# Performance work log

Hardware: AMD Instinct MI355X
Metric: run time of the kernel (lower is better)

The kernel has to match this reference:

```python
import jax, jax.numpy as jnp
import numpy as np

B, L, FT, FS, H = 32, 4096, 512, 512, 512  # batch, seq, text feat, summary feat, hidden
C = FT + FS + 1  # conv1 in-channels (num_features + 1 coverage channel)


def setup_inputs() -> dict:
    key = jax.random.key(0)
    ks = jax.random.split(key, 8)
    text_states = jax.random.normal(ks[0], (B, L, FT), dtype=jnp.float32)
    summary_current_state = jax.random.normal(ks[1], (B, FS), dtype=jnp.float32)
    coverage = jax.random.uniform(ks[2], (B, 1, L), dtype=jnp.float32)
    W1 = jax.random.normal(ks[3], (H, C), dtype=jnp.float32) * (1.0 / np.sqrt(C))
    b1 = jnp.zeros((H,), dtype=jnp.float32)
    W2 = jax.random.normal(ks[4], (1, H), dtype=jnp.float32) * (1.0 / np.sqrt(H))
    b2 = jnp.zeros((1,), dtype=jnp.float32)
    text_length = jax.random.randint(ks[5], (B,), 1, L + 1)  # >=1 so softmax is defined
    return {
        "text_states": text_states,
        "summary_current_state": summary_current_state,
        "coverage": coverage,
        "W1": W1,
        "b1": b1,
        "W2": W2,
        "b2": b2,
        "text_length": text_length,
    }


def reference(text_states, summary_current_state, coverage, W1, b1, W2, b2, text_length):
    b, l, ft = text_states.shape
    ts = jnp.swapaxes(text_states, -1, -2)  # [B, FT, L]
    ss = jnp.broadcast_to(summary_current_state[..., None],
                          summary_current_state.shape + (l,))  # [B, FS, L]
    x = jnp.concatenate([ts, ss, coverage], axis=-2)  # [B, C, L]
    # kernel-size-1 Conv1d == pointwise linear over channels
    h = jnp.tanh(jnp.einsum('bcl,hc->bhl', x, W1) + b1[None, :, None])  # [B, H, L]
    logits = jnp.einsum('bhl,oh->bol', h, W2) + b2[None, :, None]  # [B, 1, L]
    mask = jnp.arange(l)[None, None, :] < text_length[:, None, None]  # [B, 1, L]
    masked = jnp.where(mask, logits, -jnp.inf)
    attention = jax.nn.softmax(masked, axis=-1)  # [B, 1, L]
    context_vector = jnp.sum(attention * ts, axis=-1)  # [B, FT]
    return context_vector, attention
```

## Files before the change

### kernel.cpp

```cpp
#include <hip/hip_runtime.h>
#include <cstdint>
#include <cstddef>

#define B_  32
#define L_  4096
#define FT_ 512
#define FS_ 512
#define H_  512
#define C_  1025
#define TL  64
#define NCH (L_ / TL)

typedef __attribute__((ext_vector_type(8))) short short8;
typedef __attribute__((ext_vector_type(4))) float float4v;

__device__ __forceinline__ short f2bf(float f) {
    union { float f; unsigned u; } v; v.f = f;
    unsigned r = v.u + 0x7FFF + ((v.u >> 16) & 1);
    return (short)(r >> 16);
}

__device__ __forceinline__ float fast_tanh(float x) {
    float e = __expf(2.f * x);
    return 1.f - 2.f * __builtin_amdgcn_rcpf(e + 1.f);
}

__global__ __launch_bounds__(256) void prep_kernel(
        const float* __restrict__ W1, const float* __restrict__ summary,
        const float* __restrict__ b1, short* __restrict__ fragB,
        float* __restrict__ w1c, float* __restrict__ sconst) {
    if (blockIdx.x < 128) {
        int gid = blockIdx.x * 256 + threadIdx.x;
        int lane = gid & 63;
        int ts_  = gid >> 6;
        int t = ts_ >> 4;
        int s = ts_ & 15;
        int h  = t * 16 + (lane & 15);
        int k0 = s * 32 + (lane >> 4) * 8;
        const float* src = W1 + (size_t)h * C_ + k0;
        short8 o;
        #pragma unroll
        for (int j = 0; j < 8; ++j) o[j] = f2bf(src[j]);
        *(short8*)(fragB + (size_t)gid * 8) = o;
        if (gid < H_) w1c[gid] = W1[(size_t)gid * C_ + FT_ + FS_];
    } else {
        int wid  = ((blockIdx.x - 128) * 256 + threadIdx.x) >> 6;
        int lane = threadIdx.x & 63;
        int b = wid >> 9;
        int h = wid & 511;
        const float* wrow = W1 + (size_t)h * C_ + FT_;
        const float* srow = summary + (size_t)b * FS_;
        float acc = 0.f;
        #pragma unroll
        for (int f = lane; f < FS_; f += 64) acc += wrow[f] * srow[f];
        #pragma unroll
        for (int off = 32; off > 0; off >>= 1) acc += __shfl_down(acc, off, 64);
        if (lane == 0) sconst[wid] = acc + b1[h];
    }
}

__global__ __launch_bounds__(512, 4) void logits_ctx_kernel(
        const float* __restrict__ ts, const float* __restrict__ coverage,
        const int* __restrict__ text_length,
        const short* __restrict__ fragB, const float* __restrict__ w1c,
        const float* __restrict__ sconst, const float* __restrict__ W2,
        const float* __restrict__ b2, float* __restrict__ logits,
        float2* __restrict__ stats_c, float* __restrict__ cpart) {
    const int b  = blockIdx.y;
    const int l0 = blockIdx.x * TL;
    const int len = text_length[b];
    if (l0 >= len) return;

    __shared__ short ts_lds[TL * 512];

    const float4* src = (const float4*)(ts + ((size_t)b * L_ + l0) * FT_);
    for (int j = threadIdx.x; j < TL * 64; j += 512) {
        int l = j >> 6;
        int g = j & 63;
        float4 v0 = src[2 * j];
        float4 v1 = src[2 * j + 1];
        short8 p;
        p[0] = f2bf(v0.x); p[1] = f2bf(v0.y); p[2] = f2bf(v0.z); p[3] = f2bf(v0.w);
        p[4] = f2bf(v1.x); p[5] = f2bf(v1.y); p[6] = f2bf(v1.z); p[7] = f2bf(v1.w);
        *(short8*)(ts_lds + l * 512 + ((g ^ (l & 7)) << 3)) = p;
    }
    __syncthreads();

    const int lane = threadIdx.x & 63;
    const int wv   = threadIdx.x >> 6;
    const int col  = lane & 15;
    const int quad = lane >> 4;
    const int swz  = col & 7;

    const short* aBase = ts_lds + col * 512;
    const short* bBase = fragB + (size_t)(wv * 4) * 16 * 512 + lane * 8;

#define LDB(ntv, ksv) (*(const short8*)(bBase + (size_t)((ntv) * 16 + (ksv)) * 512))

    float4v acc[4][4];
    #pragma unroll
    for (int nt = 0; nt < 4; ++nt)
        #pragma unroll
        for (int mt = 0; mt < 4; ++mt)
            acc[nt][mt] = (float4v){0.f, 0.f, 0.f, 0.f};

    short8 bc0 = LDB(0, 0), bc1 = LDB(1, 0), bc2 = LDB(2, 0), bc3 = LDB(3, 0);

    for (int ks = 0; ks < 15; ++ks) {
        short8 af[4];
        const int ag = ((ks * 4 + quad) ^ swz) << 3;
        #pragma unroll
        for (int mt = 0; mt < 4; ++mt)
            af[mt] = *(const short8*)(aBase + mt * (16 * 512) + ag);
        short8 bn0 = LDB(0, ks + 1), bn1 = LDB(1, ks + 1),
               bn2 = LDB(2, ks + 1), bn3 = LDB(3, ks + 1);
        #pragma unroll
        for (int mt = 0; mt < 4; ++mt)
            acc[0][mt] = __builtin_amdgcn_mfma_f32_16x16x32_bf16(af[mt], bc0, acc[0][mt], 0, 0, 0);
        #pragma unroll
        for (int mt = 0; mt < 4; ++mt)
            acc[1][mt] = __builtin_amdgcn_mfma_f32_16x16x32_bf16(af[mt], bc1, acc[1][mt], 0, 0, 0);
        #pragma unroll
        for (int mt = 0; mt < 4; ++mt)
            acc[2][mt] = __builtin_amdgcn_mfma_f32_16x16x32_bf16(af[mt], bc2, acc[2][mt], 0, 0, 0);
        #pragma unroll
        for (int mt = 0; mt < 4; ++mt)
            acc[3][mt] = __builtin_amdgcn_mfma_f32_16x16x32_bf16(af[mt], bc3, acc[3][mt], 0, 0, 0);
        bc0 = bn0; bc1 = bn1; bc2 = bn2; bc3 = bn3;
    }
    {
        short8 af[4];
        const int ag = ((15 * 4 + quad) ^ swz) << 3;
        #pragma unroll
        for (int mt = 0; mt < 4; ++mt)
            af[mt] = *(const short8*)(aBase + mt * (16 * 512) + ag);
        #pragma unroll
        for (int mt = 0; mt < 4; ++mt)
            acc[0][mt] = __builtin_amdgcn_mfma_f32_16x16x32_bf16(af[mt], bc0, acc[0][mt], 0, 0, 0);
        #pragma unroll
        for (int mt = 0; mt < 4; ++mt)
            acc[1][mt] = __builtin_amdgcn_mfma_f32_16x16x32_bf16(af[mt], bc1, acc[1][mt], 0, 0, 0);
        #pragma unroll
        for (int mt = 0; mt < 4; ++mt)
            acc[2][mt] = __builtin_amdgcn_mfma_f32_16x16x32_bf16(af[mt], bc2, acc[2][mt], 0, 0, 0);
        #pragma unroll
        for (int mt = 0; mt < 4; ++mt)
            acc[3][mt] = __builtin_amdgcn_mfma_f32_16x16x32_bf16(af[mt], bc3, acc[3][mt], 0, 0, 0);
    }
#undef LDB

    const int h0 = wv * 64;
    const float* sc_b = sconst + (size_t)b * H_;
    float4 cov[4];
    #pragma unroll
    for (int mt = 0; mt < 4; ++mt)
        cov[mt] = *(const float4*)(coverage + (size_t)b * L_ + l0 + mt * 16 + quad * 4);

    float partial[4][4];
    #pragma unroll
    for (int mt = 0; mt < 4; ++mt)
        #pragma unroll
        for (int r = 0; r < 4; ++r) partial[mt][r] = 0.f;

    #pragma unroll
    for (int nt = 0; nt < 4; ++nt) {
        const int h = h0 + nt * 16 + col;
        const float sc = sc_b[h];
        const float wc = w1c[h];
        const float w2 = W2[h];
        #pragma unroll
        for (int mt = 0; mt < 4; ++mt)
            #pragma unroll
            for (int r = 0; r < 4; ++r) {
                float pre = acc[nt][mt][r] + sc + wc * ((const float*)&cov[mt])[r];
                partial[mt][r] += w2 * fast_tanh(pre);
            }
    }

    #pragma unroll
    for (int mt = 0; mt < 4; ++mt)
        #pragma unroll
        for (int r = 0; r < 4; ++r) {
            float v = partial[mt][r];
            v += __shfl_xor(v, 8, 64);
            v += __shfl_xor(v, 4, 64);
            v += __shfl_xor(v, 2, 64);
            v += __shfl_xor(v, 1, 64);
            partial[mt][r] = v;
        }

    __syncthreads();
    float* red  = (float*)ts_lds;
    float* wbuf = red + 512;
    if (col == 0) {
        #pragma unroll
        for (int mt = 0; mt < 4; ++mt)
            #pragma unroll
            for (int r = 0; r < 4; ++r)
                red[wv * 64 + mt * 16 + quad * 4 + r] = partial[mt][r];
    }
    __syncthreads();

    if (threadIdx.x < 64) {
        const int t = threadIdx.x;
        const bool valid = (l0 + t < len);
        float lg = b2[0];
        #pragma unroll
        for (int w = 0; w < 8; ++w) lg += red[w * 64 + t];
        logits[(size_t)b * L_ + l0 + t] = lg;
        float mv = valid ? lg : -INFINITY;
        #pragma unroll
        for (int off = 32; off > 0; off >>= 1)
            mv = fmaxf(mv, __shfl_xor(mv, off, 64));
        const float wt = valid ? __expf(lg - mv) : 0.f;
        float sv = wt;
        #pragma unroll
        for (int off = 32; off > 0; off >>= 1) sv += __shfl_xor(sv, off, 64);
        wbuf[t] = wt;
        if (t == 0) {
            float2 o; o.x = mv; o.y = sv;
            stats_c[(size_t)b * NCH + blockIdx.x] = o;
        }
    }
    __syncthreads();

    const int lend = min(len - l0, TL);
    const float* tsb = ts + ((size_t)b * L_ + l0) * FT_ + threadIdx.x;
    float cx = 0.f;
    #pragma unroll 4
    for (int l = 0; l < lend; ++l) cx += wbuf[l] * tsb[(size_t)l * FT_];
    cpart[((size_t)b * NCH + blockIdx.x) * FT_ + threadIdx.x] = cx;
}

__global__ __launch_bounds__(512) void finalize_kernel(
        const float* __restrict__ logits, const float2* __restrict__ stats_c,
        const float* __restrict__ cpart, const int* __restrict__ text_length,
        float* __restrict__ ctx, float* __restrict__ attn_out) {
    const int b   = blockIdx.x;
    const int len = text_length[b];
    const int nv  = (len + TL - 1) / TL;
    const int t   = threadIdx.x;
    __shared__ float sm[NCH];
    __shared__ float redm[8];
    __shared__ float reds[8];

    float2 st; st.x = 0.f; st.y = 0.f;
    float mloc = -INFINITY;
    if (t < nv) { st = stats_c[(size_t)b * NCH + t]; mloc = st.x; }
    float v = mloc;
    #pragma unroll
    for (int off = 32; off > 0; off >>= 1) v = fmaxf(v, __shfl_xor(v, off, 64));
    if ((t & 63) == 0) redm[t >> 6] = v;
    __syncthreads();
    float m = redm[0];
    #pragma unroll
    for (int w = 1; w < 8; ++w) m = fmaxf(m, redm[w]);

    float sume = 0.f;
    if (t < nv) {
        const float sc = __expf(st.x - m);
        sm[t] = sc;
        sume = st.y * sc;
    }
    float sv = sume;
    #pragma unroll
    for (int off = 32; off > 0; off >>= 1) sv += __shfl_xor(sv, off, 64);
    if ((t & 63) == 0) reds[t >> 6] = sv;
    __syncthreads();
    float tot = 0.f;
    #pragma unroll
    for (int w = 0; w < 8; ++w) tot += reds[w];
    const float inv = 1.f / tot;

    const float* lgrow = logits + (size_t)b * L_;
    float* arow = attn_out + (size_t)b * L_;
    #pragma unroll
    for (int i = 0; i < L_ / 512; ++i) {
        const int l = i * 512 + t;
        float a = 0.f;
        if (l < len) a = __expf(lgrow[l] - m) * inv;
        arow[l] = a;
    }

    const float* cp = cpart + (size_t)b * NCH * FT_ + t;
    float c = 0.f;
    #pragma unroll 4
    for (int ch = 0; ch < nv; ++ch) c += sm[ch] * cp[(size_t)ch * FT_];
    ctx[(size_t)b * FT_ + t] = c * inv;
}

extern "C" void kernel_launch(void* const* d_in, const int* in_sizes, int n_in,
                              void* d_out, int out_size, void* d_ws, size_t ws_size,
                              hipStream_t stream) {
    const float* ts       = (const float*)d_in[0];
    const float* summary  = (const float*)d_in[1];
    const float* coverage = (const float*)d_in[2];
    const float* W1       = (const float*)d_in[3];
    const float* b1       = (const float*)d_in[4];
    const float* W2       = (const float*)d_in[5];
    const float* b2       = (const float*)d_in[6];
    const int*   text_len = (const int*)d_in[7];

    float* ctx_out  = (float*)d_out;
    float* attn_out = (float*)d_out + B_ * FT_;

    char* ws = (char*)d_ws;
    short*  fragB   = (short*)(ws);
    float*  w1c     = (float*)(ws + 524288);
    float*  sconst  = (float*)(ws + 526336);
    float*  logits  = (float*)(ws + 591872);
    float2* stats_c = (float2*)(ws + 1116160);
    float*  cpart   = (float*)(ws + 1132544);

    prep_kernel<<<128 + 4096, 256, 0, stream>>>(W1, summary, b1, fragB, w1c, sconst);
    logits_ctx_kernel<<<dim3(NCH, B_), 512, 0, stream>>>(
        ts, coverage, text_len, fragB, w1c, sconst, W2, b2, logits, stats_c, cpart);
    finalize_kernel<<<B_, 512, 0, stream>>>(
        logits, stats_c, cpart, text_len, ctx_out, attn_out);
}
```

Baseline: 429.4 us.

## Fuse finalize into logits kernel via last-block atomic counter; batch summary dot

Removes the separate finalize launch. Each block of the logits kernel bumps a per-batch atomic counter, and the last block for a batch performs the softmax merge, attention write and context reduction. The prep kernel now has each wave compute four batches' summary projections while reusing the W1 row held in registers, cutting its grid fourfold, and it also zeroes the counters. The cost is extra fences and a serial tail inside the last block per batch, plus more LDS per block, which may affect occupancy.

```diff
diff --git a/kernel.cpp b/kernel.cpp
--- a/kernel.cpp
+++ b/kernel.cpp
@@ -28,7 +28,8 @@
 __global__ __launch_bounds__(256) void prep_kernel(
         const float* __restrict__ W1, const float* __restrict__ summary,
         const float* __restrict__ b1, short* __restrict__ fragB,
-        float* __restrict__ w1c, float* __restrict__ sconst) {
+        float* __restrict__ w1c, float* __restrict__ sconst,
+        int* __restrict__ cnt) {
     if (blockIdx.x < 128) {
         int gid = blockIdx.x * 256 + threadIdx.x;
         int lane = gid & 63;
@@ -43,19 +44,27 @@
         for (int j = 0; j < 8; ++j) o[j] = f2bf(src[j]);
         *(short8*)(fragB + (size_t)gid * 8) = o;
         if (gid < H_) w1c[gid] = W1[(size_t)gid * C_ + FT_ + FS_];
+        if (gid < B_) cnt[gid] = 0;
     } else {
         int wid  = ((blockIdx.x - 128) * 256 + threadIdx.x) >> 6;
         int lane = threadIdx.x & 63;
-        int b = wid >> 9;
-        int h = wid & 511;
+        int h  = wid & 511;
+        int bq = wid >> 9;
         const float* wrow = W1 + (size_t)h * C_ + FT_;
-        const float* srow = summary + (size_t)b * FS_;
-        float acc = 0.f;
-        #pragma unroll
-        for (int f = lane; f < FS_; f += 64) acc += wrow[f] * srow[f];
-        #pragma unroll
-        for (int off = 32; off > 0; off >>= 1) acc += __shfl_down(acc, off, 64);
-        if (lane == 0) sconst[wid] = acc + b1[h];
+        float w[8];
+        #pragma unroll
+        for (int j = 0; j < 8; ++j) w[j] = wrow[lane + 64 * j];
+        #pragma unroll
+        for (int bi = 0; bi < 4; ++bi) {
+            const int b = bq * 4 + bi;
+            const float* srow = summary + (size_t)b * FS_;
+            float acc = 0.f;
+            #pragma unroll
+            for (int j = 0; j < 8; ++j) acc += w[j] * srow[lane + 64 * j];
+            #pragma unroll
+            for (int off = 32; off > 0; off >>= 1) acc += __shfl_down(acc, off, 64);
+            if (lane == 0) sconst[(size_t)b * H_ + h] = acc + b1[h];
+        }
     }
 }
 
@@ -65,13 +74,19 @@
         const short* __restrict__ fragB, const float* __restrict__ w1c,
         const float* __restrict__ sconst, const float* __restrict__ W2,
         const float* __restrict__ b2, float* __restrict__ logits,
-        float2* __restrict__ stats_c, float* __restrict__ cpart) {
+        float2* __restrict__ stats_c, float* __restrict__ cpart,
+        int* __restrict__ cnt, float* __restrict__ ctx,
+        float* __restrict__ attn_out) {
     const int b  = blockIdx.y;
     const int l0 = blockIdx.x * TL;
     const int len = text_length[b];
     if (l0 >= len) return;
 
     __shared__ short ts_lds[TL * 512];
+    __shared__ float fin_sm[NCH];
+    __shared__ float fin_redm[8];
+    __shared__ float fin_reds[8];
+    __shared__ int   fin_flag;
 
     const float4* src = (const float4*)(ts + ((size_t)b * L_ + l0) * FT_);
     for (int j = threadIdx.x; j < TL * 64; j += 512) {
@@ -230,46 +245,45 @@
     #pragma unroll 4
     for (int l = 0; l < lend; ++l) cx += wbuf[l] * tsb[(size_t)l * FT_];
     cpart[((size_t)b * NCH + blockIdx.x) * FT_ + threadIdx.x] = cx;
-}
-
-__global__ __launch_bounds__(512) void finalize_kernel(
-        const float* __restrict__ logits, const float2* __restrict__ stats_c,
-        const float* __restrict__ cpart, const int* __restrict__ text_length,
-        float* __restrict__ ctx, float* __restrict__ attn_out) {
-    const int b   = blockIdx.x;
-    const int len = text_length[b];
-    const int nv  = (len + TL - 1) / TL;
-    const int t   = threadIdx.x;
-    __shared__ float sm[NCH];
-    __shared__ float redm[8];
-    __shared__ float reds[8];
-
+
+    const int nv = (len + TL - 1) / TL;
+    __threadfence();
+    __syncthreads();
+    if (threadIdx.x == 0) {
+        int old = atomicAdd(&cnt[b], 1);
+        fin_flag = (old == nv - 1);
+    }
+    __syncthreads();
+    if (!fin_flag) return;
+    __threadfence();
+
+    const int t = threadIdx.x;
     float2 st; st.x = 0.f; st.y = 0.f;
     float mloc = -INFINITY;
     if (t < nv) { st = stats_c[(size_t)b * NCH + t]; mloc = st.x; }
     float v = mloc;
     #pragma unroll
     for (int off = 32; off > 0; off >>= 1) v = fmaxf(v, __shfl_xor(v, off, 64));
-    if ((t & 63) == 0) redm[t >> 6] = v;
-    __syncthreads();
-    float m = redm[0];
-    #pragma unroll
-    for (int w = 1; w < 8; ++w) m = fmaxf(m, redm[w]);
+    if ((t & 63) == 0) fin_redm[t >> 6] = v;
+    __syncthreads();
+    float m = fin_redm[0];
+    #pragma unroll
+    for (int w = 1; w < 8; ++w) m = fmaxf(m, fin_redm[w]);
 
     float sume = 0.f;
     if (t < nv) {
         const float sc = __expf(st.x - m);
-        sm[t] = sc;
+        fin_sm[t] = sc;
         sume = st.y * sc;
     }
     float sv = sume;
     #pragma unroll
     for (int off = 32; off > 0; off >>= 1) sv += __shfl_xor(sv, off, 64);
-    if ((t & 63) == 0) reds[t >> 6] = sv;
+    if ((t & 63) == 0) fin_reds[t >> 6] = sv;
     __syncthreads();
     float tot = 0.f;
     #pragma unroll
-    for (int w = 0; w < 8; ++w) tot += reds[w];
+    for (int w = 0; w < 8; ++w) tot += fin_reds[w];
     const float inv = 1.f / tot;
 
     const float* lgrow = logits + (size_t)b * L_;
@@ -285,7 +299,7 @@
     const float* cp = cpart + (size_t)b * NCH * FT_ + t;
     float c = 0.f;
     #pragma unroll 4
-    for (int ch = 0; ch < nv; ++ch) c += sm[ch] * cp[(size_t)ch * FT_];
+    for (int ch = 0; ch < nv; ++ch) c += fin_sm[ch] * cp[(size_t)ch * FT_];
     ctx[(size_t)b * FT_ + t] = c * inv;
 }
 
@@ -311,10 +325,11 @@
     float*  logits  = (float*)(ws + 591872);
     float2* stats_c = (float2*)(ws + 1116160);
     float*  cpart   = (float*)(ws + 1132544);
-
-    prep_kernel<<<128 + 4096, 256, 0, stream>>>(W1, summary, b1, fragB, w1c, sconst);
+    int*    cnt     = (int*)(ws + 5326848);
+
+    prep_kernel<<<128 + 1024, 256, 0, stream>>>(W1, summary, b1, fragB, w1c,
+                                                sconst, cnt);
     logits_ctx_kernel<<<dim3(NCH, B_), 512, 0, stream>>>(
-        ts, coverage, text_len, fragB, w1c, sconst, W2, b2, logits, stats_c, cpart);
-    finalize_kernel<<<B_, 512, 0, stream>>>(
-        logits, stats_c, cpart, text_len, ctx_out, attn_out);
-}
+        ts, coverage, text_len, fragB, w1c, sconst, W2, b2, logits, stats_c,
+        cpart, cnt, ctx_out, attn_out);
+}
```

Result: slower. 763.3 us (+77.8%).
